# Performance work log

Hardware: AMD Instinct MI355X
Metric: run time of the kernel (lower is better)

## Reference

```python
import jax, jax.numpy as jnp
import numpy as np

EPS = 1e-8

def _penalty(v, lo, hi):
    # if v<lo: (lo-v)/lo ; elif v>hi (hi finite): (v-hi)/hi ; else 0
    below = (lo - v) / lo
    if np.isinf(hi):
        return jnp.where(v < lo, below, 0.0)
    above = (v - hi) / hi
    return jnp.where(v < lo, below, jnp.where(v > hi, above, 0.0))

def _symbolic_features(x):
    # x: [B, input_dim]; column mapping from the original per-row loop
    am, bod, do, ph, nit = x[:, 0], x[:, 1], x[:, 2], x[:, 4], x[:, 7]
    # penalties in param_order = [ph, ammonia, bod, dissolved_oxygen, nitrate]
    p_ph  = _penalty(ph, 6.5, 8.5)
    p_am  = _penalty(am, 0.001, 0.5)
    p_bod = _penalty(bod, 0.001, 5.0)
    p_do  = _penalty(do, 6.0, np.inf)
    p_nit = _penalty(nit, 0.001, 10.0)
    # pollutant scores (missing params like 'nitrogen'/'orthophosphate' are skipped -> count adjusts)
    s_bact = (1.2 * am / (0.5 + EPS) + 1.5 * bod / (5.0 + EPS) - 0.8 * do / (10.0 + EPS)) / 3.0
    s_chem = (1.5 * ph / (8.5 + EPS) + 1.0 * nit / (10.0 + EPS)) / 2.0
    s_org  = (2.0 * bod / (5.0 + EPS) - 1.5 * do / (10.0 + EPS) + 0.8 * am / (0.5 + EPS)) / 3.0
    s_agr  = (2.0 * nit / (10.0 + EPS)) / 1.0
    resil = 1.0 / (1.0 + (p_ph + p_am + p_bod + p_do + p_nit) + EPS)
    return jnp.stack([p_ph, p_am, p_bod, p_do, p_nit, s_bact, s_chem, s_org, s_agr, resil], axis=1)

def setup_inputs() -> dict:
    key = jax.random.key(0)
    ks = jax.random.split(key, 16)
    B, D_IN, SYM, H = 1048576, 10, 10, 64
    def lin(k, fin, fout):
        k1, k2 = jax.random.split(k)
        s = 1.0 / np.sqrt(fin)
        return (jax.random.uniform(k1, (fin, fout), jnp.float32, -s, s),
                jax.random.uniform(k2, (fout,), jnp.float32, -s, s))
    W_sym, b_sym = lin(ks[0], SYM, H // 2)
    W_in, b_in = lin(ks[1], D_IN + H // 2, H)
    W1, b1 = lin(ks[2], H, H)
    W2, b2 = lin(ks[3], H, H)
    W3, b3 = lin(ks[4], H, H)
    W_r1, b_r1 = lin(ks[5], H, H // 2)
    W_r2, b_r2 = lin(ks[6], H // 2, 1)
    W_c1, b_c1 = lin(ks[7], H, H // 2)
    W_c2, b_c2 = lin(ks[8], H // 2, 4)
    x = jax.random.uniform(ks[9], (B, D_IN), jnp.float32)
    return {"x": x, "W_sym": W_sym, "b_sym": b_sym, "W_in": W_in, "b_in": b_in,
            "W1": W1, "b1": b1, "W2": W2, "b2": b2, "W3": W3, "b3": b3,
            "W_r1": W_r1, "b_r1": b_r1, "W_r2": W_r2, "b_r2": b_r2,
            "W_c1": W_c1, "b_c1": b_c1, "W_c2": W_c2, "b_c2": b_c2}

def reference(x, W_sym, b_sym, W_in, b_in, W1, b1, W2, b2, W3, b3,
              W_r1, b_r1, W_r2, b_r2, W_c1, b_c1, W_c2, b_c2):
    elu = jax.nn.elu
    sym = _symbolic_features(x)                      # [B, 10]
    sym_enc = elu(sym @ W_sym + b_sym)               # [B, 32]  (Dropout: eval mode = identity)
    h = elu(jnp.concatenate([x, sym_enc], axis=1) @ W_in + b_in)  # [B, 64]
    for W, b in ((W1, b1), (W2, b2), (W3, b3)):
        h = h + elu(h @ W + b)                       # residual MLP stack
    predictions = elu(h @ W_r1 + b_r1) @ W_r2 + b_r2            # [B, 1]
    pollutant_logits = elu(h @ W_c1 + b_c1) @ W_c2 + b_c2       # [B, 4]
    return predictions, pollutant_logits
```

## Files before the change

### kernel.cpp

```cpp
#include <hip/hip_runtime.h>
#include <hip/hip_bf16.h>
#include <math.h>

#define NROWS 1048576
#define EPSF 1e-8f
#define GRID 512
#define TPB 256
#define ITERS 16

typedef unsigned short ushortT;
typedef __attribute__((ext_vector_type(8))) short short8;
typedef __attribute__((ext_vector_type(4))) short short4v;
typedef __attribute__((ext_vector_type(4))) float floatx4;
typedef __attribute__((ext_vector_type(2))) int int2v;

#define WS_HI   256
#define WS_LO   41216
#define WS_MF   82176
#define MF_B5   0
#define MF_WSYM 320
#define MF_BSYM 640
#define MF_WR2  672
#define MF_BR2  704
#define MF_WC2  708
#define MF_BC2  836
#define MF_WC2T 840
#define MF_TOTAL 968

#define LDS_FENCE() asm volatile("s_waitcnt lgkmcnt(0)" ::: "memory")

struct WPtrs { const void* p[19]; };

__global__ void sniff_kernel(const ushortT* __restrict__ x, int* __restrict__ flag) {
    if (threadIdx.x == 0 && blockIdx.x == 0) {
        unsigned s = 0;
        for (int i = 0; i < 64; ++i) s |= (unsigned)(x[i] & 0x8000u);
        *flag = s ? 1 : 0;
    }
}

__device__ __forceinline__ float ldw(const void* p, int i, bool f32) {
    return f32 ? ((const float*)p)[i]
               : __uint_as_float(((unsigned)((const ushortT*)p)[i]) << 16);
}

__global__ void prep_kernel(WPtrs wp, const int* __restrict__ flag, void* __restrict__ ws) {
    const bool f32 = (*flag != 0);
    ushortT* hi = (ushortT*)((char*)ws + WS_HI);
    ushortT* lo = (ushortT*)((char*)ws + WS_LO);
    float* mf = (float*)((char*)ws + WS_MF);
    const int B = blockIdx.x;
    if (B < 5) {
        const int L = B;
        for (int idx = threadIdx.x; idx < 4096; idx += 256) {
            const int j8 = idx & 7, ln = (idx >> 3) & 63, s2 = (idx >> 9) & 1, t = idx >> 10;
            const int s = 2 * s2 + (j8 >> 2), j = j8 & 3;
            const int k = 16 * s + 4 * (ln >> 4) + j;
            const int m = 16 * t + (ln & 15);
            float w = 0.0f;
            if (L == 0)      { if (k < 42) w = ldw(wp.p[3], k * 64 + m, f32); }
            else if (L <= 3) { if (k < 64) w = ldw(wp.p[3 + 2 * L], k * 64 + m, f32); }
            else             { if (k < 64) w = (m < 32) ? ldw(wp.p[11], k * 32 + m, f32)
                                                        : ldw(wp.p[15], k * 32 + (m - 32), f32); }
            const unsigned u = __float_as_uint(w);
            const float rem = w - __uint_as_float(u & 0xffff0000u);
            hi[L * 4096 + idx] = (ushortT)(u >> 16);
            lo[L * 4096 + idx] = (ushortT)(__float_as_uint(rem) >> 16);
        }
    } else {
        const int src[12] = {4, 6, 8, 10, 12, 16, 1, 2, 13, 14, 17, 18};
        const int cnt[12] = {64, 64, 64, 64, 32, 32, 320, 32, 32, 1, 128, 4};
        const int dst[12] = {0, 64, 128, 192, 256, 288, MF_WSYM, MF_BSYM, MF_WR2, MF_BR2, MF_WC2, MF_BC2};
        for (int a = 0; a < 12; ++a)
            for (int i = threadIdx.x; i < cnt[a]; i += 256)
                mf[dst[a] + i] = ldw(wp.p[src[a]], i, f32);
        for (int i = threadIdx.x; i < 128; i += 256) {
            const int qq = i >> 5, j = i & 31;
            mf[MF_WC2T + i] = ldw(wp.p[17], j * 4 + qq, f32);
        }
    }
}

__device__ __forceinline__ float eluf(float v) {
    return fmaxf(v, 0.0f) + (__expf(fminf(v, 0.0f)) - 1.0f);
}

__device__ __forceinline__ unsigned pack_hi16(unsigned ua, unsigned ub) {
    return __builtin_amdgcn_perm(ub, ua, 0x07060302u);
}

__device__ __forceinline__ void split4(float a0, float a1, float a2, float a3,
                                       short4v& h4, short4v& l4) {
    const unsigned u0 = __float_as_uint(a0), u1 = __float_as_uint(a1);
    const unsigned u2 = __float_as_uint(a2), u3 = __float_as_uint(a3);
    int2v h, l;
    h[0] = (int)pack_hi16(u0, u1);
    h[1] = (int)pack_hi16(u2, u3);
    const float l0 = a0 - __uint_as_float(u0 & 0xffff0000u);
    const float l1 = a1 - __uint_as_float(u1 & 0xffff0000u);
    const float l2 = a2 - __uint_as_float(u2 & 0xffff0000u);
    const float l3 = a3 - __uint_as_float(u3 & 0xffff0000u);
    l[0] = (int)pack_hi16(__float_as_uint(l0), __float_as_uint(l1));
    l[1] = (int)pack_hi16(__float_as_uint(l2), __float_as_uint(l3));
    h4 = __builtin_bit_cast(short4v, h);
    l4 = __builtin_bit_cast(short4v, l);
}

__device__ __forceinline__ floatx4 mfma16(short4v a, short4v b, floatx4 c) {
#if __has_builtin(__builtin_amdgcn_mfma_f32_16x16x16bf16_1k)
    return __builtin_amdgcn_mfma_f32_16x16x16bf16_1k(a, b, c, 0, 0, 0);
#else
    floatx4 d;
    asm("v_mfma_f32_16x16x16_bf16 %0, %1, %2, %3" : "=v"(d) : "v"(a), "v"(b), "v"(c));
    return d;
#endif
}

template<bool F32>
__device__ __forceinline__ void run_body(
    const void* __restrict__ xin, const char* __restrict__ wsb,
    void* __restrict__ out,
    const ushortT* __restrict__ wlds,
    const float* __restrict__ mflds,
    float (* __restrict__ hb)[68],
    const int lane, const int wavebase)
{
    const ushortT* __restrict__ wflo = (const ushortT*)(wsb + WS_LO);
    const int n = lane & 15, q = lane >> 4;

    #pragma unroll
    for (int i = 0; i < 6; ++i) {
        const int c = 42 + q * 6 + i;
        if (c < 64) hb[n][c] = 0.0f;
    }

    unsigned xu[2][5];
    float xf[2][10];
    #pragma unroll
    for (int u = 0; u < 2; ++u) {
        const int rowg = wavebase + 16 * u + n;
        if (F32) {
            const float* xp = (const float*)xin + (size_t)rowg * 10;
            #pragma unroll
            for (int i = 0; i < 10; ++i) xf[u][i] = xp[i];
        } else {
            const unsigned* xd = (const unsigned*)((const ushortT*)xin + (size_t)rowg * 10);
            #pragma unroll
            for (int i = 0; i < 5; ++i) xu[u][i] = xd[i];
        }
    }

    #pragma unroll 1
    for (int it = 0; it < ITERS; ++it) {
        const int rowbase = wavebase + it * 32;
        short4v Bhi[2][4], Blo[2][4];

        #pragma unroll
        for (int u = 0; u < 2; ++u) {
            float x[10];
            if (F32) {
                #pragma unroll
                for (int i = 0; i < 10; ++i) x[i] = xf[u][i];
            } else {
                #pragma unroll
                for (int i = 0; i < 5; ++i) {
                    const unsigned d = xu[u][i];
                    x[2 * i]     = __uint_as_float(d << 16);
                    x[2 * i + 1] = __uint_as_float(d & 0xffff0000u);
                }
            }
            if (q == 0) {
                #pragma unroll
                for (int i = 0; i < 10; ++i) hb[n][i] = x[i];
            }

            const float am = x[0], bod = x[1], dox = x[2], ph = x[4], nit = x[7];
            const float p_ph  = ph  < 6.5f   ? (6.5f - ph) * 0.15384616f
                              : (ph > 8.5f   ? (ph - 8.5f) * 0.11764706f : 0.0f);
            const float p_am  = am  < 0.001f ? (0.001f - am) * 1000.0f
                              : (am > 0.5f   ? (am - 0.5f) * 2.0f : 0.0f);
            const float p_bod = bod < 0.001f ? (0.001f - bod) * 1000.0f
                              : (bod > 5.0f  ? (bod - 5.0f) * 0.2f : 0.0f);
            const float p_do  = dox < 6.0f   ? (6.0f - dox) * 0.16666667f : 0.0f;
            const float p_nit = nit < 0.001f ? (0.001f - nit) * 1000.0f
                              : (nit > 10.0f ? (nit - 10.0f) * 0.1f : 0.0f);
            const float s_bact = (am * 2.3999999f + bod * 0.29999998f - dox * 0.08f) * 0.33333334f;
            const float s_chem = (ph * 0.17647059f + nit * 0.1f) * 0.5f;
            const float s_org  = (bod * 0.39999998f - dox * 0.14999999f + am * 1.5999999f) * 0.33333334f;
            const float s_agr  = nit * 0.2f;
            const float resil  = 1.0f / (1.0f + (p_ph + p_am + p_bod + p_do + p_nit) + EPSF);
            const float sym[10] = {p_ph, p_am, p_bod, p_do, p_nit, s_bact, s_chem, s_org, s_agr, resil};

            float se[8];
            {
                const floatx4 b0 = *(const floatx4*)(mflds + MF_BSYM + q * 8);
                const floatx4 b1 = *(const floatx4*)(mflds + MF_BSYM + q * 8 + 4);
                #pragma unroll
                for (int jj = 0; jj < 4; ++jj) { se[jj] = b0[jj]; se[4 + jj] = b1[jj]; }
                #pragma unroll
                for (int k = 0; k < 10; ++k) {
                    const floatx4 w0 = *(const floatx4*)(mflds + MF_WSYM + k * 32 + q * 8);
                    const floatx4 w1 = *(const floatx4*)(mflds + MF_WSYM + k * 32 + q * 8 + 4);
                    #pragma unroll
                    for (int jj = 0; jj < 4; ++jj) {
                        se[jj]     = fmaf(sym[k], w0[jj], se[jj]);
                        se[4 + jj] = fmaf(sym[k], w1[jj], se[4 + jj]);
                    }
                }
            }
            #pragma unroll
            for (int jj = 0; jj < 8; ++jj) hb[n][10 + q * 8 + jj] = eluf(se[jj]);
            LDS_FENCE();
            #pragma unroll
            for (int s = 0; s < 4; ++s) {
                const floatx4 v = *(const floatx4*)&hb[n][16 * s + 4 * q];
                split4(v[0], v[1], v[2], v[3], Bhi[u][s], Blo[u][s]);
            }
            LDS_FENCE();
        }

        {
            const int itn = (it + 1 < ITERS) ? it + 1 : it;
            #pragma unroll
            for (int u = 0; u < 2; ++u) {
                const int rowg = wavebase + itn * 32 + 16 * u + n;
                if (F32) {
                    const float* xp = (const float*)xin + (size_t)rowg * 10;
                    #pragma unroll
                    for (int i = 0; i < 10; ++i) xf[u][i] = xp[i];
                } else {
                    const unsigned* xd = (const unsigned*)((const ushortT*)xin + (size_t)rowg * 10);
                    #pragma unroll
                    for (int i = 0; i < 5; ++i) xu[u][i] = xd[i];
                }
            }
        }

        float hprev[2][4][4];
        #pragma unroll
        for (int L = 0; L < 5; ++L) {
            short8 Ap[8];
            const ushortT* wl = wlds + L * 4096 + lane * 8;
            #pragma unroll
            for (int c = 0; c < 8; ++c)
                Ap[c] = *(const short8*)(wl + c * 512);
            short8 Alp[8];
            if (F32) {
                const int base = L * 4096 + lane * 8;
                #pragma unroll
                for (int c = 0; c < 8; ++c)
                    Alp[c] = *(const short8*)(wflo + base + c * 512);
            }

            floatx4 acc[2][4];
            #pragma unroll
            for (int t = 0; t < 4; ++t) {
                const floatx4 b = *(const floatx4*)(mflds + MF_B5 + L * 64 + 16 * t + 4 * q);
                acc[0][t] = b; acc[1][t] = b;
            }
            #pragma unroll
            for (int t = 0; t < 4; ++t) {
                #pragma unroll
                for (int s2 = 0; s2 < 2; ++s2) {
                    const short8 A = Ap[t * 2 + s2];
                    const short4v ae = {A[0], A[1], A[2], A[3]};
                    const short4v ao = {A[4], A[5], A[6], A[7]};
                    #pragma unroll
                    for (int u = 0; u < 2; ++u) {
                        acc[u][t] = mfma16(ae, Bhi[u][2 * s2],     acc[u][t]);
                        acc[u][t] = mfma16(ae, Blo[u][2 * s2],     acc[u][t]);
                        acc[u][t] = mfma16(ao, Bhi[u][2 * s2 + 1], acc[u][t]);
                        acc[u][t] = mfma16(ao, Blo[u][2 * s2 + 1], acc[u][t]);
                    }
                    if (F32) {
                        const short8 Al = Alp[t * 2 + s2];
                        const short4v le  = {Al[0], Al[1], Al[2], Al[3]};
                        const short4v lo_ = {Al[4], Al[5], Al[6], Al[7]};
                        #pragma unroll
                        for (int u = 0; u < 2; ++u) {
                            acc[u][t] = mfma16(le,  Bhi[u][2 * s2],     acc[u][t]);
                            acc[u][t] = mfma16(lo_, Bhi[u][2 * s2 + 1], acc[u][t]);
                        }
                    }
                }
            }

            if (L < 4) {
                #pragma unroll
                for (int u = 0; u < 2; ++u) {
                    #pragma unroll
                    for (int t = 0; t < 4; ++t) {
                        #pragma unroll
                        for (int r = 0; r < 4; ++r) {
                            float e = eluf(acc[u][t][r]);
                            if (L >= 1) e += hprev[u][t][r];
                            hprev[u][t][r] = e;
                        }
                        split4(hprev[u][t][0], hprev[u][t][1],
                               hprev[u][t][2], hprev[u][t][3], Bhi[u][t], Blo[u][t]);
                    }
                }
            } else {
                const floatx4 wr0 = *(const floatx4*)(mflds + MF_WR2 + 4 * q);
                const floatx4 wr1 = *(const floatx4*)(mflds + MF_WR2 + 16 + 4 * q);
                #pragma unroll
                for (int u = 0; u < 2; ++u) {
                    float pred = (q == 0) ? mflds[MF_BR2] : 0.0f;
                    float z2[4], z3[4];
                    #pragma unroll
                    for (int r = 0; r < 4; ++r) {
                        pred = fmaf(eluf(acc[u][0][r]), wr0[r], pred);
                        pred = fmaf(eluf(acc[u][1][r]), wr1[r], pred);
                        z2[r] = eluf(acc[u][2][r]);
                        z3[r] = eluf(acc[u][3][r]);
                    }
                    float lg[4];
                    #pragma unroll
                    for (int c = 0; c < 4; ++c) {
                        const floatx4 wc0 = *(const floatx4*)(mflds + MF_WC2T + c * 32 + 4 * q);
                        const floatx4 wc1 = *(const floatx4*)(mflds + MF_WC2T + c * 32 + 16 + 4 * q);
                        float l = (q == 0) ? mflds[MF_BC2 + c] : 0.0f;
                        #pragma unroll
                        for (int r = 0; r < 4; ++r) {
                            l = fmaf(z2[r], wc0[r], l);
                            l = fmaf(z3[r], wc1[r], l);
                        }
                        lg[c] = l;
                    }
                    pred += __shfl_xor(pred, 16, 64);
                    pred += __shfl_xor(pred, 32, 64);
                    #pragma unroll
                    for (int c = 0; c < 4; ++c) {
                        lg[c] += __shfl_xor(lg[c], 16, 64);
                        lg[c] += __shfl_xor(lg[c], 32, 64);
                    }
                    const float lsel = q == 0 ? lg[0] : (q == 1 ? lg[1] : (q == 2 ? lg[2] : lg[3]));
                    const int rowg = rowbase + 16 * u + n;
                    if (F32) {
                        float* o = (float*)out;
                        if (q == 0) o[rowg] = pred;
                        o[NROWS + rowg * 4 + q] = lsel;
                    } else {
                        __hip_bfloat16* o = (__hip_bfloat16*)out;
                        if (q == 0) o[rowg] = __float2bfloat16(pred);
                        o[NROWS + rowg * 4 + q] = __float2bfloat16(lsel);
                    }
                }
            }
        }
    }
}

__global__ __launch_bounds__(TPB, 2) void mlp_mfma_kernel(
    const void* __restrict__ xin, const int* __restrict__ flagp,
    const void* __restrict__ ws, void* __restrict__ out)
{
    __shared__ __align__(16) ushortT wlds[5 * 4096];
    __shared__ __align__(16) float mflds[MF_TOTAL];
    __shared__ float hball[4][16][68];

    const int tid = threadIdx.x;
    {
        const unsigned* src = (const unsigned*)((const char*)ws + WS_HI);
        unsigned* dst = (unsigned*)wlds;
        for (int i = tid; i < 10240; i += TPB) dst[i] = src[i];
        const float* mfsrc = (const float*)((const char*)ws + WS_MF);
        for (int i = tid; i < MF_TOTAL; i += TPB) mflds[i] = mfsrc[i];
    }
    __syncthreads();

    const int wave = tid >> 6, lane = tid & 63;
    const int gw = blockIdx.x * 4 + wave;
    const int wavebase = gw * (32 * ITERS);
    if (*flagp != 0)
        run_body<true>(xin, (const char*)ws, out, wlds, mflds, hball[wave], lane, wavebase);
    else
        run_body<false>(xin, (const char*)ws, out, wlds, mflds, hball[wave], lane, wavebase);
}

extern "C" void kernel_launch(void* const* d_in, const int* in_sizes, int n_in,
                              void* d_out, int out_size, void* d_ws, size_t ws_size,
                              hipStream_t stream) {
    (void)in_sizes; (void)n_in; (void)out_size; (void)ws_size;
    int* flag = (int*)d_ws;

    sniff_kernel<<<1, 64, 0, stream>>>((const ushortT*)d_in[0], flag);

    WPtrs wp;
    for (int i = 0; i < 19; ++i) wp.p[i] = d_in[i];
    prep_kernel<<<6, 256, 0, stream>>>(wp, flag, d_ws);

    mlp_mfma_kernel<<<GRID, TPB, 0, stream>>>(d_in[0], flag, d_ws, d_out);
}
```

Before: 334.3 us.

## Move symbolic encoder to MFMA and drop LDS staging of layer-0 input

Computes the 10->32 symbolic encoder with bf16 hi/lo MFMA instead of scalar FMAs, and builds the layer-0 B operands straight from registers, which removes the per-wave LDS scratch buffer and its fences. The layer-0 weight rows are reordered so the sym-encoder outputs come first and the raw x columns follow, which lets the zero-padded K slice skip some MFMAs. The residual is rebuilt from the packed hi/lo values rather than kept in a separate float array, freeing registers. Blocks grow to 512 threads with 4 blocks per CU and half the iterations per wave. Risks are register pressure under the new launch bounds and a small precision change from the hi+lo reconstruction of the residual.

```diff
diff --git a/kernel.cpp b/kernel.cpp
--- a/kernel.cpp
+++ b/kernel.cpp
@@ -5,8 +5,8 @@
 #define NROWS 1048576
 #define EPSF 1e-8f
 #define GRID 512
-#define TPB 256
-#define ITERS 16
+#define TPB 512
+#define ITERS 8
 
 typedef unsigned short ushortT;
 typedef __attribute__((ext_vector_type(8))) short short8;
@@ -14,9 +14,11 @@
 typedef __attribute__((ext_vector_type(4))) float floatx4;
 typedef __attribute__((ext_vector_type(2))) int int2v;
 
+#define WE_OFF  20480
+#define WTAB    20992
 #define WS_HI   256
-#define WS_LO   41216
-#define WS_MF   82176
+#define WS_LO   (256 + WTAB * 2)
+#define WS_MF   (WS_LO + WTAB * 2)
 #define MF_B5   0
 #define MF_WSYM 320
 #define MF_BSYM 640
@@ -26,8 +28,6 @@
 #define MF_BC2  836
 #define MF_WC2T 840
 #define MF_TOTAL 968
-
-#define LDS_FENCE() asm volatile("s_waitcnt lgkmcnt(0)" ::: "memory")
 
 struct WPtrs { const void* p[19]; };
 
@@ -58,7 +58,10 @@
             const int k = 16 * s + 4 * (ln >> 4) + j;
             const int m = 16 * t + (ln & 15);
             float w = 0.0f;
-            if (L == 0)      { if (k < 42) w = ldw(wp.p[3], k * 64 + m, f32); }
+            if (L == 0) {
+                const int ksrc = (k < 32) ? (10 + k) : (k < 42 ? k - 32 : -1);
+                if (ksrc >= 0) w = ldw(wp.p[3], ksrc * 64 + m, f32);
+            }
             else if (L <= 3) { if (k < 64) w = ldw(wp.p[3 + 2 * L], k * 64 + m, f32); }
             else             { if (k < 64) w = (m < 32) ? ldw(wp.p[11], k * 32 + m, f32)
                                                         : ldw(wp.p[15], k * 32 + (m - 32), f32); }
@@ -68,6 +71,16 @@
             lo[L * 4096 + idx] = (ushortT)(__float_as_uint(rem) >> 16);
         }
     } else {
+        for (int idx = threadIdx.x; idx < 512; idx += 256) {
+            const int j = idx & 3, ln = (idx >> 2) & 63, t = idx >> 8;
+            const int k = 4 * (ln >> 4) + j;
+            const int m = 16 * t + (ln & 15);
+            const float w = (k < 10) ? ldw(wp.p[1], k * 32 + m, f32) : 0.0f;
+            const unsigned u = __float_as_uint(w);
+            const float rem = w - __uint_as_float(u & 0xffff0000u);
+            hi[WE_OFF + idx] = (ushortT)(u >> 16);
+            lo[WE_OFF + idx] = (ushortT)(__float_as_uint(rem) >> 16);
+        }
         const int src[12] = {4, 6, 8, 10, 12, 16, 1, 2, 13, 14, 17, 18};
         const int cnt[12] = {64, 64, 64, 64, 32, 32, 320, 32, 32, 1, 128, 4};
         const int dst[12] = {0, 64, 128, 192, 256, 288, MF_WSYM, MF_BSYM, MF_WR2, MF_BR2, MF_WC2, MF_BC2};
@@ -87,6 +100,10 @@
 
 __device__ __forceinline__ unsigned pack_hi16(unsigned ua, unsigned ub) {
     return __builtin_amdgcn_perm(ub, ua, 0x07060302u);
+}
+
+__device__ __forceinline__ float b2f(short h) {
+    return __uint_as_float(((unsigned)(ushortT)h) << 16);
 }
 
 __device__ __forceinline__ void split4(float a0, float a1, float a2, float a3,
@@ -122,17 +139,10 @@
     void* __restrict__ out,
     const ushortT* __restrict__ wlds,
     const float* __restrict__ mflds,
-    float (* __restrict__ hb)[68],
     const int lane, const int wavebase)
 {
     const ushortT* __restrict__ wflo = (const ushortT*)(wsb + WS_LO);
     const int n = lane & 15, q = lane >> 4;
-
-    #pragma unroll
-    for (int i = 0; i < 6; ++i) {
-        const int c = 42 + q * 6 + i;
-        if (c < 64) hb[n][c] = 0.0f;
-    }
 
     unsigned xu[2][5];
     float xf[2][10];
@@ -168,10 +178,6 @@
                     x[2 * i]     = __uint_as_float(d << 16);
                     x[2 * i + 1] = __uint_as_float(d & 0xffff0000u);
                 }
-            }
-            if (q == 0) {
-                #pragma unroll
-                for (int i = 0; i < 10; ++i) hb[n][i] = x[i];
             }
 
             const float am = x[0], bod = x[1], dox = x[2], ph = x[4], nit = x[7];
@@ -189,34 +195,43 @@
             const float s_org  = (bod * 0.39999998f - dox * 0.14999999f + am * 1.5999999f) * 0.33333334f;
             const float s_agr  = nit * 0.2f;
             const float resil  = 1.0f / (1.0f + (p_ph + p_am + p_bod + p_do + p_nit) + EPSF);
-            const float sym[10] = {p_ph, p_am, p_bod, p_do, p_nit, s_bact, s_chem, s_org, s_agr, resil};
-
-            float se[8];
-            {
-                const floatx4 b0 = *(const floatx4*)(mflds + MF_BSYM + q * 8);
-                const floatx4 b1 = *(const floatx4*)(mflds + MF_BSYM + q * 8 + 4);
-                #pragma unroll
-                for (int jj = 0; jj < 4; ++jj) { se[jj] = b0[jj]; se[4 + jj] = b1[jj]; }
-                #pragma unroll
-                for (int k = 0; k < 10; ++k) {
-                    const floatx4 w0 = *(const floatx4*)(mflds + MF_WSYM + k * 32 + q * 8);
-                    const floatx4 w1 = *(const floatx4*)(mflds + MF_WSYM + k * 32 + q * 8 + 4);
-                    #pragma unroll
-                    for (int jj = 0; jj < 4; ++jj) {
-                        se[jj]     = fmaf(sym[k], w0[jj], se[jj]);
-                        se[4 + jj] = fmaf(sym[k], w1[jj], se[4 + jj]);
-                    }
-                }
-            }
-            #pragma unroll
-            for (int jj = 0; jj < 8; ++jj) hb[n][10 + q * 8 + jj] = eluf(se[jj]);
-            LDS_FENCE();
-            #pragma unroll
-            for (int s = 0; s < 4; ++s) {
-                const floatx4 v = *(const floatx4*)&hb[n][16 * s + 4 * q];
-                split4(v[0], v[1], v[2], v[3], Bhi[u][s], Blo[u][s]);
-            }
-            LDS_FENCE();
+
+            const float sv0 = q == 0 ? p_ph  : q == 1 ? p_nit  : q == 2 ? s_agr : 0.0f;
+            const float sv1 = q == 0 ? p_am  : q == 1 ? s_bact : q == 2 ? resil : 0.0f;
+            const float sv2 = q == 0 ? p_bod : q == 1 ? s_chem : 0.0f;
+            const float sv3 = q == 0 ? p_do  : q == 1 ? s_org  : 0.0f;
+            short4v SymH, SymL;
+            split4(sv0, sv1, sv2, sv3, SymH, SymL);
+
+            #pragma unroll
+            for (int t = 0; t < 2; ++t) {
+                floatx4 ae_acc = *(const floatx4*)(mflds + MF_BSYM + 16 * t + 4 * q);
+                const short4v Ae = *(const short4v*)(wlds + WE_OFF + t * 256 + lane * 4);
+                ae_acc = mfma16(Ae, SymH, ae_acc);
+                ae_acc = mfma16(Ae, SymL, ae_acc);
+                if (F32) {
+                    const short4v Al = *(const short4v*)(wflo + WE_OFF + t * 256 + lane * 4);
+                    ae_acc = mfma16(Al, SymH, ae_acc);
+                }
+                split4(eluf(ae_acc[0]), eluf(ae_acc[1]), eluf(ae_acc[2]), eluf(ae_acc[3]),
+                       Bhi[u][t], Blo[u][t]);
+            }
+
+            if (F32) {
+                const float v0 = q == 0 ? x[0] : q == 1 ? x[4] : q == 2 ? x[8] : 0.0f;
+                const float v1 = q == 0 ? x[1] : q == 1 ? x[5] : q == 2 ? x[9] : 0.0f;
+                const float v2 = q == 0 ? x[2] : q == 1 ? x[6] : 0.0f;
+                const float v3 = q == 0 ? x[3] : q == 1 ? x[7] : 0.0f;
+                split4(v0, v1, v2, v3, Bhi[u][2], Blo[u][2]);
+            } else {
+                int2v xd;
+                xd[0] = (int)(q == 0 ? xu[u][0] : q == 1 ? xu[u][2] : q == 2 ? xu[u][4] : 0u);
+                xd[1] = (int)(q == 0 ? xu[u][1] : q == 1 ? xu[u][3] : 0u);
+                Bhi[u][2] = __builtin_bit_cast(short4v, xd);
+                Blo[u][2] = (short4v){0, 0, 0, 0};
+            }
+            Bhi[u][3] = (short4v){0, 0, 0, 0};
+            Blo[u][3] = (short4v){0, 0, 0, 0};
         }
 
         {
@@ -236,7 +251,6 @@
             }
         }
 
-        float hprev[2][4][4];
         #pragma unroll
         for (int L = 0; L < 5; ++L) {
             short8 Ap[8];
@@ -265,22 +279,35 @@
                     const short8 A = Ap[t * 2 + s2];
                     const short4v ae = {A[0], A[1], A[2], A[3]};
                     const short4v ao = {A[4], A[5], A[6], A[7]};
-                    #pragma unroll
-                    for (int u = 0; u < 2; ++u) {
-                        acc[u][t] = mfma16(ae, Bhi[u][2 * s2],     acc[u][t]);
-                        acc[u][t] = mfma16(ae, Blo[u][2 * s2],     acc[u][t]);
-                        acc[u][t] = mfma16(ao, Bhi[u][2 * s2 + 1], acc[u][t]);
-                        acc[u][t] = mfma16(ao, Blo[u][2 * s2 + 1], acc[u][t]);
-                    }
-                    if (F32) {
-                        const short8 Al = Alp[t * 2 + s2];
-                        const short4v le  = {Al[0], Al[1], Al[2], Al[3]};
-                        const short4v lo_ = {Al[4], Al[5], Al[6], Al[7]};
+                    if (L == 0 && s2 == 1) {
                         #pragma unroll
                         for (int u = 0; u < 2; ++u) {
-                            acc[u][t] = mfma16(le,  Bhi[u][2 * s2],     acc[u][t]);
-                            acc[u][t] = mfma16(lo_, Bhi[u][2 * s2 + 1], acc[u][t]);
+                            acc[u][t] = mfma16(ae, Bhi[u][2], acc[u][t]);
+                            if (F32) {
+                                acc[u][t] = mfma16(ae, Blo[u][2], acc[u][t]);
+                                const short8 Al = Alp[t * 2 + s2];
+                                const short4v le = {Al[0], Al[1], Al[2], Al[3]};
+                                acc[u][t] = mfma16(le, Bhi[u][2], acc[u][t]);
+                            }
                         }
+                    } else {
+                        #pragma unroll
+                        for (int u = 0; u < 2; ++u) {
+                            acc[u][t] = mfma16(ae, Bhi[u][2 * s2],     acc[u][t]);
+                            acc[u][t] = mfma16(ae, Blo[u][2 * s2],     acc[u][t]);
+                            acc[u][t] = mfma16(ao, Bhi[u][2 * s2 + 1], acc[u][t]);
+                            acc[u][t] = mfma16(ao, Blo[u][2 * s2 + 1], acc[u][t]);
+                        }
+                        if (F32) {
+                            const short8 Al = Alp[t * 2 + s2];
+                            const short4v le  = {Al[0], Al[1], Al[2], Al[3]};
+                            const short4v lo_ = {Al[4], Al[5], Al[6], Al[7]};
+                            #pragma unroll
+                            for (int u = 0; u < 2; ++u) {
+                                acc[u][t] = mfma16(le,  Bhi[u][2 * s2],     acc[u][t]);
+                                acc[u][t] = mfma16(lo_, Bhi[u][2 * s2 + 1], acc[u][t]);
+                            }
+                        }
                     }
                 }
             }
@@ -290,14 +317,14 @@
                 for (int u = 0; u < 2; ++u) {
                     #pragma unroll
                     for (int t = 0; t < 4; ++t) {
+                        float h[4];
                         #pragma unroll
                         for (int r = 0; r < 4; ++r) {
                             float e = eluf(acc[u][t][r]);
-                            if (L >= 1) e += hprev[u][t][r];
-                            hprev[u][t][r] = e;
+                            if (L >= 1) e += b2f(Bhi[u][t][r]) + b2f(Blo[u][t][r]);
+                            h[r] = e;
                         }
-                        split4(hprev[u][t][0], hprev[u][t][1],
-                               hprev[u][t][2], hprev[u][t][3], Bhi[u][t], Blo[u][t]);
+                        split4(h[0], h[1], h[2], h[3], Bhi[u][t], Blo[u][t]);
                     }
                 }
             } else {
@@ -351,31 +378,30 @@
     }
 }
 
-__global__ __launch_bounds__(TPB, 2) void mlp_mfma_kernel(
+__global__ __launch_bounds__(TPB, 4) void mlp_mfma_kernel(
     const void* __restrict__ xin, const int* __restrict__ flagp,
     const void* __restrict__ ws, void* __restrict__ out)
 {
-    __shared__ __align__(16) ushortT wlds[5 * 4096];
+    __shared__ __align__(16) ushortT wlds[WTAB];
     __shared__ __align__(16) float mflds[MF_TOTAL];
-    __shared__ float hball[4][16][68];
 
     const int tid = threadIdx.x;
     {
         const unsigned* src = (const unsigned*)((const char*)ws + WS_HI);
         unsigned* dst = (unsigned*)wlds;
-        for (int i = tid; i < 10240; i += TPB) dst[i] = src[i];
+        for (int i = tid; i < WTAB / 2; i += TPB) dst[i] = src[i];
         const float* mfsrc = (const float*)((const char*)ws + WS_MF);
         for (int i = tid; i < MF_TOTAL; i += TPB) mflds[i] = mfsrc[i];
     }
     __syncthreads();
 
     const int wave = tid >> 6, lane = tid & 63;
-    const int gw = blockIdx.x * 4 + wave;
+    const int gw = blockIdx.x * (TPB / 64) + wave;
     const int wavebase = gw * (32 * ITERS);
     if (*flagp != 0)
-        run_body<true>(xin, (const char*)ws, out, wlds, mflds, hball[wave], lane, wavebase);
+        run_body<true>(xin, (const char*)ws, out, wlds, mflds, lane, wavebase);
     else
-        run_body<false>(xin, (const char*)ws, out, wlds, mflds, hball[wave], lane, wavebase);
+        run_body<false>(xin, (const char*)ws, out, wlds, mflds, lane, wavebase);
 }
 
 extern "C" void kernel_launch(void* const* d_in, const int* in_sizes, int n_in,
```

Result: slower. 1.033 ms (+209.0%).
